# Optimization experiments

Measured on AMD Instinct MI355X. Metric: run time of the kernel, lower is better.

The kernel has to match this reference:

```python
import jax, jax.numpy as jnp
import numpy as np

D_MODEL = 512
N_HEADS = 8
D_K = D_MODEL // N_HEADS
B, L_Q, L_K = 4, 2048, 2048


def setup_inputs() -> dict:
    key = jax.random.key(0)
    ks = jax.random.split(key, 13)
    s = 1.0 / np.sqrt(D_MODEL)
    return {
        "Q_in": jax.random.normal(ks[0], (B, L_Q, D_MODEL), jnp.float32),
        "K_in": jax.random.normal(ks[1], (B, L_K, D_MODEL), jnp.float32),
        "V_in": jax.random.normal(ks[2], (B, L_K, D_MODEL), jnp.float32),
        "M": jax.random.uniform(ks[3], (N_HEADS, L_Q, L_K), jnp.float32),
        "Wq": jax.random.uniform(ks[4], (D_MODEL, D_MODEL), jnp.float32, -s, s),
        "bq": jnp.zeros((D_MODEL,), jnp.float32),
        "Wk": jax.random.uniform(ks[5], (D_MODEL, D_MODEL), jnp.float32, -s, s),
        "bk": jnp.zeros((D_MODEL,), jnp.float32),
        "Wv": jax.random.uniform(ks[6], (D_MODEL, D_MODEL), jnp.float32, -s, s),
        "bv": jnp.zeros((D_MODEL,), jnp.float32),
        "Wo": jax.random.uniform(ks[7], (D_MODEL, D_MODEL), jnp.float32, -s, s),
        "bo": jnp.zeros((D_MODEL,), jnp.float32),
        "logit_alpha": jnp.zeros((N_HEADS,), jnp.float32),
    }


def reference(Q_in, K_in, V_in, M, Wq, bq, Wk, bk, Wv, bv, Wo, bo, logit_alpha):
    b, lq, _ = Q_in.shape
    lk = K_in.shape[1]
    # projections (torch Linear: x @ W.T + b), split into heads: [b, h, l, d_k]
    Q = (Q_in @ Wq.T + bq).reshape(b, lq, N_HEADS, D_K).transpose(0, 2, 1, 3)
    K = (K_in @ Wk.T + bk).reshape(b, lk, N_HEADS, D_K).transpose(0, 2, 1, 3)
    V = (V_in @ Wv.T + bv).reshape(b, lk, N_HEADS, D_K).transpose(0, 2, 1, 3)
    logits = jnp.einsum("bhqd,bhkd->bhqk", Q, K) / jnp.sqrt(jnp.asarray(D_K, Q.dtype))
    attn = jax.nn.softmax(logits, axis=-1)
    alpha = jax.nn.sigmoid(logit_alpha)[None, :, None, None]  # [1, h, 1, 1]
    gate = alpha * M[None] + (1.0 - alpha)  # post-softmax soft-mask gate
    attn = attn * gate
    out = jnp.einsum("bhqk,bhkd->bqhd", attn, V).reshape(b, lq, D_MODEL)
    return out @ Wo.T + bo, attn
```

## Files before the change

### kernel.cpp

```cpp
#include <hip/hip_runtime.h>
#include <hip/hip_bf16.h>

typedef unsigned short u16;
typedef unsigned int u32;
typedef short bf16x8 __attribute__((ext_vector_type(8)));
typedef float f32x4 __attribute__((ext_vector_type(4)));
typedef u16 u16x8 __attribute__((ext_vector_type(8)));
typedef u32 u32x2 __attribute__((ext_vector_type(2)));

#define WQ_ 0
#define WK_ 262144
#define WV_ 524288
#define WO_ 786432
#define QP_ 1048576
#define KP_ (QP_ + 4194304)
#define VT_ (KP_ + 4194304)
#define OW_ (VT_ + 4194304)

#define C1F 0.18033688011112042f

__device__ __forceinline__ u16 f2bf(float f) {
  unsigned x = __float_as_uint(f);
  return (u16)((x + 0x7fffu + ((x >> 16) & 1u)) >> 16);
}

__device__ __forceinline__ u32 packbf2(float a, float b) {
  u32 lo = (u32)__bfloat16_as_ushort(__float2bfloat16(a));
  u32 hi = (u32)__bfloat16_as_ushort(__float2bfloat16(b));
  return lo | (hi << 16);
}

__device__ __forceinline__ void async16(const void* g, void* l) {
  __builtin_amdgcn_global_load_lds(
      (const __attribute__((address_space(1))) unsigned int*)g,
      (__attribute__((address_space(3))) unsigned int*)l, 16, 0, 0);
}

__global__ void convert_w(const float* __restrict__ Wq, const float* __restrict__ Wk,
                          const float* __restrict__ Wv, const float* __restrict__ Wo,
                          u16* __restrict__ ws) {
  int seg = blockIdx.y;
  const float* src = (seg == 0) ? Wq : (seg == 1) ? Wk : (seg == 2) ? Wv : Wo;
  u16* dst = ws + seg * 262144;
  int i = (blockIdx.x * 256 + threadIdx.x) * 8;
  float4 a = *(const float4*)(src + i);
  float4 b = *(const float4*)(src + i + 4);
  u16x8 o;
  o[0] = f2bf(a.x); o[1] = f2bf(a.y); o[2] = f2bf(a.z); o[3] = f2bf(a.w);
  o[4] = f2bf(b.x); o[5] = f2bf(b.y); o[6] = f2bf(b.z); o[7] = f2bf(b.w);
  *(u16x8*)(dst + i) = o;
}

template <int MODE>
__global__ __launch_bounds__(256, 3) void gemm_nt(
    const float* __restrict__ A0, const float* __restrict__ A1,
    const float* __restrict__ A2, u16* __restrict__ ws,
    const float* __restrict__ bias0, const float* __restrict__ bias1,
    const float* __restrict__ bias2, float* __restrict__ outF) {
  const int tid = threadIdx.x, lane = tid & 63, wave = tid >> 6;
  const int wm = wave >> 1, wn = wave & 1;
  const int z = blockIdx.z;
  const float* Af = (z == 0) ? A0 : (z == 1) ? A1 : A2;
  const u16* W = ws + (MODE == 0 ? z * 262144 : (int)WO_);
  const u16* Ab = ws + OW_;
  const float* bias = (z == 0) ? bias0 : (z == 1) ? bias1 : bias2;
  const int bm0 = blockIdx.y * 128, bn0 = blockIdx.x * 128;

  __shared__ u16 At[8192];
  __shared__ u16 Bt[8192];

  f32x4 acc[4][4];
#pragma unroll
  for (int i = 0; i < 4; ++i)
#pragma unroll
    for (int j = 0; j < 4; ++j) acc[i][j] = (f32x4){0.f, 0.f, 0.f, 0.f};

  const int grp16 = (lane >> 4) * 16;

  for (int kt = 0; kt < 8; ++kt) {
    __syncthreads();
#pragma unroll
    for (int c = 0; c < 4; ++c) {
      int o = wave * 4096 + c * 1024 + lane * 16;
      int row = o >> 7;
      int colb = (o & 127) ^ ((row & 7) << 4);
      async16((const char*)W + (size_t)(bn0 + row) * 1024 + kt * 128 + colb,
              (char*)Bt + wave * 4096 + c * 1024);
      if (MODE == 1) {
        async16((const char*)Ab + (size_t)(bm0 + row) * 1024 + kt * 128 + colb,
                (char*)At + wave * 4096 + c * 1024);
      }
    }
    if (MODE == 0) {
#pragma unroll
      for (int i = 0; i < 4; ++i) {
        int c = tid + 256 * i;
        int row = c >> 3, fc = (c & 7) * 8;
        const float* s = Af + (size_t)(bm0 + row) * 512 + kt * 64 + fc;
        f32x4 x0 = *(const f32x4*)s;
        f32x4 x1 = *(const f32x4*)(s + 4);
        u16x8 p;
        p[0] = __bfloat16_as_ushort(__float2bfloat16(x0[0]));
        p[1] = __bfloat16_as_ushort(__float2bfloat16(x0[1]));
        p[2] = __bfloat16_as_ushort(__float2bfloat16(x0[2]));
        p[3] = __bfloat16_as_ushort(__float2bfloat16(x0[3]));
        p[4] = __bfloat16_as_ushort(__float2bfloat16(x1[0]));
        p[5] = __bfloat16_as_ushort(__float2bfloat16(x1[1]));
        p[6] = __bfloat16_as_ushort(__float2bfloat16(x1[2]));
        p[7] = __bfloat16_as_ushort(__float2bfloat16(x1[3]));
        int db = row * 128 + ((fc * 2) ^ ((row & 7) << 4));
        *(u16x8*)((char*)At + db) = p;
      }
    }
    __syncthreads();
    bf16x8 af[4][2], bfr[4][2];
#pragma unroll
    for (int rb = 0; rb < 4; ++rb) {
      int row = wm * 64 + rb * 16 + (lane & 15);
      const char* base = (const char*)At + row * 128;
      int sw = (row & 7) << 4;
      af[rb][0] = *(const bf16x8*)(base + (grp16 ^ sw));
      af[rb][1] = *(const bf16x8*)(base + ((64 + grp16) ^ sw));
    }
#pragma unroll
    for (int cb = 0; cb < 4; ++cb) {
      int row = wn * 64 + cb * 16 + (lane & 15);
      const char* base = (const char*)Bt + row * 128;
      int sw = (row & 7) << 4;
      bfr[cb][0] = *(const bf16x8*)(base + (grp16 ^ sw));
      bfr[cb][1] = *(const bf16x8*)(base + ((64 + grp16) ^ sw));
    }
#pragma unroll
    for (int rb = 0; rb < 4; ++rb)
#pragma unroll
      for (int cb = 0; cb < 4; ++cb) {
        acc[rb][cb] = __builtin_amdgcn_mfma_f32_16x16x32_bf16(af[rb][0], bfr[cb][0],
                                                              acc[rb][cb], 0, 0, 0);
        acc[rb][cb] = __builtin_amdgcn_mfma_f32_16x16x32_bf16(af[rb][1], bfr[cb][1],
                                                              acc[rb][cb], 0, 0, 0);
      }
  }

#pragma unroll
  for (int rb = 0; rb < 4; ++rb) {
#pragma unroll
    for (int cb = 0; cb < 4; ++cb) {
      int col = bn0 + wn * 64 + cb * 16 + (lane & 15);
      float bvl = bias[col];
#pragma unroll
      for (int r = 0; r < 4; ++r) {
        int rr = bm0 + wm * 64 + rb * 16 + (lane >> 4) * 4 + r;
        float v = acc[rb][cb][r] + bvl;
        if (MODE == 1) {
          outF[(size_t)rr * 512 + col] = v;
        } else {
          int b = rr >> 11, q = rr & 2047, hh = col >> 6, dd = col & 63;
          int bh = (b << 3) | hh;
          if (z == 0) {
            ws[QP_ + (size_t)(bh * 2048 + q) * 64 + dd] = f2bf(v * C1F);
          } else if (z == 1) {
            ws[KP_ + (size_t)(bh * 2048 + q) * 64 + dd] = f2bf(v);
          } else {
            ws[VT_ + (size_t)bh * 131072 + (size_t)dd * 2048 + q] = f2bf(v);
          }
        }
      }
    }
  }
}

__global__ __launch_bounds__(256, 4) void attn_kernel(u16* __restrict__ ws,
                                                      const float* __restrict__ Mg,
                                                      const float* __restrict__ la,
                                                      float* __restrict__ attnOut) {
  const int tid = threadIdx.x, lane = tid & 63, wv = tid >> 6;
  const int colLane = lane & 15, grp = lane >> 4;
  const int yb = blockIdx.y, h = yb >> 2, b = yb & 3, bh = b * 8 + h;
  const int q0 = blockIdx.x * 64;
  const u16* Qp = ws + QP_ + (size_t)bh * 131072;
  const u16* Kp = ws + KP_ + (size_t)bh * 131072;
  const u16* Vtg = ws + VT_ + (size_t)bh * 131072;
  const float* Mh = Mg + (size_t)h * 4194304;
  float alpha = 1.f / (1.f + __expf(-la[h]));
  float oma = 1.f - alpha;

  __shared__ u16 Kt[2][4096];
  __shared__ u16 Vt[2][4096];
  __shared__ u16 Pl[4096];

  const int grp16 = grp * 16;

  bf16x8 qa0, qa1;
  {
    const u16* qb = Qp + (size_t)(q0 + wv * 16 + colLane) * 64;
    qa0 = *(const bf16x8*)(qb + grp * 8);
    qa1 = *(const bf16x8*)(qb + 32 + grp * 8);
  }

  auto stageK = [&](int buf, int kt) {
#pragma unroll
    for (int c = 0; c < 2; ++c) {
      int o = (wv * 2 + c) * 1024 + lane * 16;
      int srcb = o ^ (((o >> 7) & 7) << 4);
      async16((const char*)Kp + kt * 8192 + srcb,
              (char*)(Kt[buf]) + (wv * 2 + c) * 1024);
    }
  };
  auto stageV = [&](int buf, int kt) {
#pragma unroll
    for (int c = 0; c < 2; ++c) {
      int o = (wv * 2 + c) * 1024 + lane * 16;
      int d = o >> 7;
      int kb2 = (o & 127) ^ ((d & 7) << 4);
      async16((const char*)Vtg + (size_t)d * 4096 + kt * 128 + kb2,
              (char*)(Vt[buf]) + (wv * 2 + c) * 1024);
    }
  };
  auto qk = [&](const u16* Ktc, float sc[4][4]) {
#pragma unroll
    for (int cb = 0; cb < 4; ++cb) {
      int row = cb * 16 + colLane;
      const char* kb = (const char*)Ktc + row * 128;
      int sw = (row & 7) << 4;
      bf16x8 k0 = *(const bf16x8*)(kb + (grp16 ^ sw));
      bf16x8 k1 = *(const bf16x8*)(kb + ((64 + grp16) ^ sw));
      f32x4 a = (f32x4){0.f, 0.f, 0.f, 0.f};
      a = __builtin_amdgcn_mfma_f32_16x16x32_bf16(k0, qa0, a, 0, 0, 0);
      a = __builtin_amdgcn_mfma_f32_16x16x32_bf16(k1, qa1, a, 0, 0, 0);
#pragma unroll
      for (int r = 0; r < 4; ++r) sc[cb][r] = a[r];
    }
  };

  float zp = 0.f;
  stageK(0, 0);
  __syncthreads();
  int cur = 0;
  for (int kt = 0; kt < 32; ++kt) {
    if (kt < 31) stageK(cur ^ 1, kt + 1);
    float sc[4][4];
    qk(Kt[cur], sc);
#pragma unroll
    for (int cb = 0; cb < 4; ++cb)
#pragma unroll
      for (int r = 0; r < 4; ++r) zp += exp2f(sc[cb][r]);
    __syncthreads();
    cur ^= 1;
  }
  zp += __shfl_xor(zp, 16);
  zp += __shfl_xor(zp, 32);
  float invZ = 1.f / zp;
  float aZ = alpha * invZ, oZ = oma * invZ;

  f32x4 oacc[4];
#pragma unroll
  for (int d = 0; d < 4; ++d) oacc[d] = (f32x4){0.f, 0.f, 0.f, 0.f};

  const int qg = q0 + wv * 16 + colLane;
  const float* Mr = Mh + (size_t)qg * 2048 + grp * 4;
  float* Ar = attnOut + ((size_t)(bh * 2048 + qg)) * 2048 + grp * 4;
  char* pb = (char*)Pl + wv * 2048 + colLane * 128;
  const int psw = (colLane & 7) << 4;

  stageK(0, 0);
  stageV(0, 0);
  __syncthreads();
  cur = 0;
  for (int kt = 0; kt < 32; ++kt) {
    if (kt < 31) { stageK(cur ^ 1, kt + 1); stageV(cur ^ 1, kt + 1); }
    const float* Mk = Mr + kt * 64;
    float4 mreg[4];
#pragma unroll
    for (int cb = 0; cb < 4; ++cb) mreg[cb] = *(const float4*)(Mk + cb * 16);
    float sc[4][4];
    qk(Kt[cur], sc);
    float* Ak = Ar + kt * 64;
#pragma unroll
    for (int cb = 0; cb < 4; ++cb) {
      f32x4 uv;
      uv[0] = exp2f(sc[cb][0]) * fmaf(aZ, mreg[cb].x, oZ);
      uv[1] = exp2f(sc[cb][1]) * fmaf(aZ, mreg[cb].y, oZ);
      uv[2] = exp2f(sc[cb][2]) * fmaf(aZ, mreg[cb].z, oZ);
      uv[3] = exp2f(sc[cb][3]) * fmaf(aZ, mreg[cb].w, oZ);
      __builtin_nontemporal_store(uv, (f32x4*)(Ak + cb * 16));
      u32x2 pv;
      pv[0] = packbf2(uv[0], uv[1]);
      pv[1] = packbf2(uv[2], uv[3]);
      *(u32x2*)(pb + ((cb * 32 + grp * 8) ^ psw)) = pv;
    }
    bf16x8 pa0 = *(const bf16x8*)(pb + (grp16 ^ psw));
    bf16x8 pa1 = *(const bf16x8*)(pb + ((64 + grp16) ^ psw));
    const u16* Vtc = Vt[cur];
#pragma unroll
    for (int db = 0; db < 4; ++db) {
      int dcol = db * 16 + colLane;
      const char* vb = (const char*)Vtc + dcol * 128;
      int sw = (dcol & 7) << 4;
      bf16x8 v0 = *(const bf16x8*)(vb + (grp16 ^ sw));
      bf16x8 v1 = *(const bf16x8*)(vb + ((64 + grp16) ^ sw));
      oacc[db] = __builtin_amdgcn_mfma_f32_16x16x32_bf16(pa0, v0, oacc[db], 0, 0, 0);
      oacc[db] = __builtin_amdgcn_mfma_f32_16x16x32_bf16(pa1, v1, oacc[db], 0, 0, 0);
    }
    __syncthreads();
    cur ^= 1;
  }

#pragma unroll
  for (int db = 0; db < 4; ++db) {
    int dcol = db * 16 + colLane;
#pragma unroll
    for (int r = 0; r < 4; ++r) {
      int qq = q0 + wv * 16 + grp * 4 + r;
      ws[OW_ + (size_t)(b * 2048 + qq) * 512 + h * 64 + dcol] = f2bf(oacc[db][r]);
    }
  }
}

extern "C" void kernel_launch(void* const* d_in, const int* in_sizes, int n_in,
                              void* d_out, int out_size, void* d_ws, size_t ws_size,
                              hipStream_t stream) {
  const float* Qi = (const float*)d_in[0];
  const float* Ki = (const float*)d_in[1];
  const float* Vi = (const float*)d_in[2];
  const float* M = (const float*)d_in[3];
  const float* Wq = (const float*)d_in[4];
  const float* bq = (const float*)d_in[5];
  const float* Wk = (const float*)d_in[6];
  const float* bk = (const float*)d_in[7];
  const float* Wv = (const float*)d_in[8];
  const float* bv = (const float*)d_in[9];
  const float* Wo = (const float*)d_in[10];
  const float* bo = (const float*)d_in[11];
  const float* la = (const float*)d_in[12];
  u16* ws = (u16*)d_ws;
  float* outMain = (float*)d_out;
  float* outAttn = outMain + 4194304;

  convert_w<<<dim3(128, 4), 256, 0, stream>>>(Wq, Wk, Wv, Wo, ws);
  gemm_nt<0><<<dim3(4, 64, 3), 256, 0, stream>>>(Qi, Ki, Vi, ws, bq, bk, bv, nullptr);
  attn_kernel<<<dim3(32, 32), 256, 0, stream>>>(ws, M, la, outAttn);
  gemm_nt<1><<<dim3(4, 64, 1), 256, 0, stream>>>(nullptr, nullptr, nullptr, ws, bo,
                                                 nullptr, nullptr, outMain);
}
```

Baseline: 239.0 us.

## Split softmax denominator pass into separate larger-tile kernel and prefetch mask

Moves the first pass over K (computing the per-row softmax denominator) out of the attention kernel into a dedicated z_kernel. That kernel uses 512-thread blocks covering 128 queries with 128-key tiles, so each K tile staged into shared memory is reused across more queries, and it writes row sums to a workspace buffer. The attention kernel reads these sums and also software-prefetches the next mask tile into registers one iteration ahead. The cost is an extra kernel launch, a workspace round trip for Z, and more registers held live for the prefetched mask.

```diff
diff --git a/kernel.cpp b/kernel.cpp
--- a/kernel.cpp
+++ b/kernel.cpp
@@ -16,6 +16,7 @@
 #define KP_ (QP_ + 4194304)
 #define VT_ (KP_ + 4194304)
 #define OW_ (VT_ + 4194304)
+#define ZB_ (OW_ + 4194304)
 
 #define C1F 0.18033688011112042f
 
@@ -169,7 +170,61 @@
   }
 }
 
+__global__ __launch_bounds__(512, 2) void z_kernel(u16* __restrict__ ws,
+                                                   float* __restrict__ zb) {
+  const int tid = threadIdx.x, lane = tid & 63, wv = tid >> 6;
+  const int colLane = lane & 15, grp = lane >> 4;
+  const int bh = blockIdx.y;
+  const int q0 = blockIdx.x * 128;
+  const u16* Qp = ws + QP_ + (size_t)bh * 131072;
+  const u16* Kp = ws + KP_ + (size_t)bh * 131072;
+  __shared__ u16 Kt[2][8192];
+  const int grp16 = grp * 16;
+
+  bf16x8 qa0, qa1;
+  {
+    const u16* qb = Qp + (size_t)(q0 + wv * 16 + colLane) * 64;
+    qa0 = *(const bf16x8*)(qb + grp * 8);
+    qa1 = *(const bf16x8*)(qb + 32 + grp * 8);
+  }
+  auto stage = [&](int buf, int kt) {
+#pragma unroll
+    for (int c = 0; c < 2; ++c) {
+      int o = (c * 512 + tid) * 16;
+      int row = o >> 7;
+      int colb = (o & 127) ^ ((row & 7) << 4);
+      async16((const char*)Kp + kt * 16384 + row * 128 + colb,
+              (char*)(Kt[buf]) + o);
+    }
+  };
+  float zp = 0.f;
+  stage(0, 0);
+  __syncthreads();
+  int cur = 0;
+  for (int kt = 0; kt < 16; ++kt) {
+    if (kt < 15) stage(cur ^ 1, kt + 1);
+#pragma unroll
+    for (int cb = 0; cb < 8; ++cb) {
+      int row = cb * 16 + colLane;
+      const char* kb = (const char*)(Kt[cur]) + row * 128;
+      int sw = (row & 7) << 4;
+      bf16x8 k0 = *(const bf16x8*)(kb + (grp16 ^ sw));
+      bf16x8 k1 = *(const bf16x8*)(kb + ((64 + grp16) ^ sw));
+      f32x4 a = (f32x4){0.f, 0.f, 0.f, 0.f};
+      a = __builtin_amdgcn_mfma_f32_16x16x32_bf16(k0, qa0, a, 0, 0, 0);
+      a = __builtin_amdgcn_mfma_f32_16x16x32_bf16(k1, qa1, a, 0, 0, 0);
+      zp += exp2f(a[0]) + exp2f(a[1]) + exp2f(a[2]) + exp2f(a[3]);
+    }
+    __syncthreads();
+    cur ^= 1;
+  }
+  zp += __shfl_xor(zp, 16);
+  zp += __shfl_xor(zp, 32);
+  if (lane < 16) zb[(size_t)bh * 2048 + q0 + wv * 16 + colLane] = zp;
+}
+
 __global__ __launch_bounds__(256, 4) void attn_kernel(u16* __restrict__ ws,
+                                                      const float* __restrict__ zb,
                                                       const float* __restrict__ Mg,
                                                       const float* __restrict__ la,
                                                       float* __restrict__ attnOut) {
@@ -197,6 +252,10 @@
     qa1 = *(const bf16x8*)(qb + 32 + grp * 8);
   }
 
+  const int qg = q0 + wv * 16 + colLane;
+  float invZ = 1.f / zb[(size_t)bh * 2048 + qg];
+  float aZ = alpha * invZ, oZ = oma * invZ;
+
   auto stageK = [&](int buf, int kt) {
 #pragma unroll
     for (int c = 0; c < 2; ++c) {
@@ -232,56 +291,41 @@
     }
   };
 
-  float zp = 0.f;
-  stageK(0, 0);
-  __syncthreads();
-  int cur = 0;
-  for (int kt = 0; kt < 32; ++kt) {
-    if (kt < 31) stageK(cur ^ 1, kt + 1);
-    float sc[4][4];
-    qk(Kt[cur], sc);
-#pragma unroll
-    for (int cb = 0; cb < 4; ++cb)
-#pragma unroll
-      for (int r = 0; r < 4; ++r) zp += exp2f(sc[cb][r]);
-    __syncthreads();
-    cur ^= 1;
-  }
-  zp += __shfl_xor(zp, 16);
-  zp += __shfl_xor(zp, 32);
-  float invZ = 1.f / zp;
-  float aZ = alpha * invZ, oZ = oma * invZ;
-
   f32x4 oacc[4];
 #pragma unroll
   for (int d = 0; d < 4; ++d) oacc[d] = (f32x4){0.f, 0.f, 0.f, 0.f};
 
-  const int qg = q0 + wv * 16 + colLane;
   const float* Mr = Mh + (size_t)qg * 2048 + grp * 4;
   float* Ar = attnOut + ((size_t)(bh * 2048 + qg)) * 2048 + grp * 4;
   char* pb = (char*)Pl + wv * 2048 + colLane * 128;
   const int psw = (colLane & 7) << 4;
 
+  float4 mcur[4], mnxt[4];
+#pragma unroll
+  for (int cb = 0; cb < 4; ++cb) mcur[cb] = *(const float4*)(Mr + cb * 16);
+
   stageK(0, 0);
   stageV(0, 0);
   __syncthreads();
-  cur = 0;
+  int cur = 0;
   for (int kt = 0; kt < 32; ++kt) {
     if (kt < 31) { stageK(cur ^ 1, kt + 1); stageV(cur ^ 1, kt + 1); }
-    const float* Mk = Mr + kt * 64;
-    float4 mreg[4];
-#pragma unroll
-    for (int cb = 0; cb < 4; ++cb) mreg[cb] = *(const float4*)(Mk + cb * 16);
+    {
+      int ktn = (kt < 31) ? kt + 1 : 31;
+      const float* Mk = Mr + ktn * 64;
+#pragma unroll
+      for (int cb = 0; cb < 4; ++cb) mnxt[cb] = *(const float4*)(Mk + cb * 16);
+    }
     float sc[4][4];
     qk(Kt[cur], sc);
     float* Ak = Ar + kt * 64;
 #pragma unroll
     for (int cb = 0; cb < 4; ++cb) {
       f32x4 uv;
-      uv[0] = exp2f(sc[cb][0]) * fmaf(aZ, mreg[cb].x, oZ);
-      uv[1] = exp2f(sc[cb][1]) * fmaf(aZ, mreg[cb].y, oZ);
-      uv[2] = exp2f(sc[cb][2]) * fmaf(aZ, mreg[cb].z, oZ);
-      uv[3] = exp2f(sc[cb][3]) * fmaf(aZ, mreg[cb].w, oZ);
+      uv[0] = exp2f(sc[cb][0]) * fmaf(aZ, mcur[cb].x, oZ);
+      uv[1] = exp2f(sc[cb][1]) * fmaf(aZ, mcur[cb].y, oZ);
+      uv[2] = exp2f(sc[cb][2]) * fmaf(aZ, mcur[cb].z, oZ);
+      uv[3] = exp2f(sc[cb][3]) * fmaf(aZ, mcur[cb].w, oZ);
       __builtin_nontemporal_store(uv, (f32x4*)(Ak + cb * 16));
       u32x2 pv;
       pv[0] = packbf2(uv[0], uv[1]);
@@ -301,6 +345,8 @@
       oacc[db] = __builtin_amdgcn_mfma_f32_16x16x32_bf16(pa0, v0, oacc[db], 0, 0, 0);
       oacc[db] = __builtin_amdgcn_mfma_f32_16x16x32_bf16(pa1, v1, oacc[db], 0, 0, 0);
     }
+#pragma unroll
+    for (int cb = 0; cb < 4; ++cb) mcur[cb] = mnxt[cb];
     __syncthreads();
     cur ^= 1;
   }
@@ -333,12 +379,14 @@
   const float* bo = (const float*)d_in[11];
   const float* la = (const float*)d_in[12];
   u16* ws = (u16*)d_ws;
+  float* zb = (float*)(ws + ZB_);
   float* outMain = (float*)d_out;
   float* outAttn = outMain + 4194304;
 
   convert_w<<<dim3(128, 4), 256, 0, stream>>>(Wq, Wk, Wv, Wo, ws);
   gemm_nt<0><<<dim3(4, 64, 3), 256, 0, stream>>>(Qi, Ki, Vi, ws, bq, bk, bv, nullptr);
-  attn_kernel<<<dim3(32, 32), 256, 0, stream>>>(ws, M, la, outAttn);
+  z_kernel<<<dim3(16, 32), 512, 0, stream>>>(ws, zb);
+  attn_kernel<<<dim3(32, 32), 256, 0, stream>>>(ws, zb, M, la, outAttn);
   gemm_nt<1><<<dim3(4, 64, 1), 256, 0, stream>>>(nullptr, nullptr, nullptr, ws, bo,
                                                  nullptr, nullptr, outMain);
 }
```

New measurement: 269.2 us. +12.6%, slower.

## Load K and V fragments directly from global memory, dropping LDS staging

Applied to the files above, without the earlier changes.

Removes the double-buffered async LDS staging of K and V tiles along with the per-iteration block barriers. Each wave now loads its own MFMA operand fragments straight from global memory into registers. This drops barrier synchronisation and LDS traffic, but each of the four waves refetches the same K/V data and loses cross-wave sharing, which puts more load on L1/L2. The kernel is dominated by writing the attention matrix and reading the mask, so K/V reads may not be the bottleneck.

```diff
diff --git a/kernel.cpp b/kernel.cpp
--- a/kernel.cpp
+++ b/kernel.cpp
@@ -184,8 +184,6 @@
   float alpha = 1.f / (1.f + __expf(-la[h]));
   float oma = 1.f - alpha;
 
-  __shared__ u16 Kt[2][4096];
-  __shared__ u16 Vt[2][4096];
   __shared__ u16 Pl[4096];
 
   const int grp16 = grp * 16;
@@ -197,55 +195,32 @@
     qa1 = *(const bf16x8*)(qb + 32 + grp * 8);
   }
 
-  auto stageK = [&](int buf, int kt) {
-#pragma unroll
-    for (int c = 0; c < 2; ++c) {
-      int o = (wv * 2 + c) * 1024 + lane * 16;
-      int srcb = o ^ (((o >> 7) & 7) << 4);
-      async16((const char*)Kp + kt * 8192 + srcb,
-              (char*)(Kt[buf]) + (wv * 2 + c) * 1024);
+  auto qk = [&](int kt, float sc[4][4]) {
+    bf16x8 k0[4], k1[4];
+#pragma unroll
+    for (int cb = 0; cb < 4; ++cb) {
+      const u16* kb = Kp + (size_t)(kt * 64 + cb * 16 + colLane) * 64 + grp * 8;
+      k0[cb] = *(const bf16x8*)kb;
+      k1[cb] = *(const bf16x8*)(kb + 32);
+    }
+#pragma unroll
+    for (int cb = 0; cb < 4; ++cb) {
+      f32x4 a = (f32x4){0.f, 0.f, 0.f, 0.f};
+      a = __builtin_amdgcn_mfma_f32_16x16x32_bf16(k0[cb], qa0, a, 0, 0, 0);
+      a = __builtin_amdgcn_mfma_f32_16x16x32_bf16(k1[cb], qa1, a, 0, 0, 0);
+#pragma unroll
+      for (int r = 0; r < 4; ++r) sc[cb][r] = a[r];
     }
   };
-  auto stageV = [&](int buf, int kt) {
-#pragma unroll
-    for (int c = 0; c < 2; ++c) {
-      int o = (wv * 2 + c) * 1024 + lane * 16;
-      int d = o >> 7;
-      int kb2 = (o & 127) ^ ((d & 7) << 4);
-      async16((const char*)Vtg + (size_t)d * 4096 + kt * 128 + kb2,
-              (char*)(Vt[buf]) + (wv * 2 + c) * 1024);
-    }
-  };
-  auto qk = [&](const u16* Ktc, float sc[4][4]) {
-#pragma unroll
-    for (int cb = 0; cb < 4; ++cb) {
-      int row = cb * 16 + colLane;
-      const char* kb = (const char*)Ktc + row * 128;
-      int sw = (row & 7) << 4;
-      bf16x8 k0 = *(const bf16x8*)(kb + (grp16 ^ sw));
-      bf16x8 k1 = *(const bf16x8*)(kb + ((64 + grp16) ^ sw));
-      f32x4 a = (f32x4){0.f, 0.f, 0.f, 0.f};
-      a = __builtin_amdgcn_mfma_f32_16x16x32_bf16(k0, qa0, a, 0, 0, 0);
-      a = __builtin_amdgcn_mfma_f32_16x16x32_bf16(k1, qa1, a, 0, 0, 0);
-#pragma unroll
-      for (int r = 0; r < 4; ++r) sc[cb][r] = a[r];
-    }
-  };
 
   float zp = 0.f;
-  stageK(0, 0);
-  __syncthreads();
-  int cur = 0;
   for (int kt = 0; kt < 32; ++kt) {
-    if (kt < 31) stageK(cur ^ 1, kt + 1);
     float sc[4][4];
-    qk(Kt[cur], sc);
+    qk(kt, sc);
 #pragma unroll
     for (int cb = 0; cb < 4; ++cb)
 #pragma unroll
       for (int r = 0; r < 4; ++r) zp += exp2f(sc[cb][r]);
-    __syncthreads();
-    cur ^= 1;
   }
   zp += __shfl_xor(zp, 16);
   zp += __shfl_xor(zp, 32);
@@ -262,18 +237,13 @@
   char* pb = (char*)Pl + wv * 2048 + colLane * 128;
   const int psw = (colLane & 7) << 4;
 
-  stageK(0, 0);
-  stageV(0, 0);
-  __syncthreads();
-  cur = 0;
   for (int kt = 0; kt < 32; ++kt) {
-    if (kt < 31) { stageK(cur ^ 1, kt + 1); stageV(cur ^ 1, kt + 1); }
     const float* Mk = Mr + kt * 64;
     float4 mreg[4];
 #pragma unroll
     for (int cb = 0; cb < 4; ++cb) mreg[cb] = *(const float4*)(Mk + cb * 16);
     float sc[4][4];
-    qk(Kt[cur], sc);
+    qk(kt, sc);
     float* Ak = Ar + kt * 64;
 #pragma unroll
     for (int cb = 0; cb < 4; ++cb) {
@@ -290,19 +260,18 @@
     }
     bf16x8 pa0 = *(const bf16x8*)(pb + (grp16 ^ psw));
     bf16x8 pa1 = *(const bf16x8*)(pb + ((64 + grp16) ^ psw));
-    const u16* Vtc = Vt[cur];
+    bf16x8 v0[4], v1[4];
 #pragma unroll
     for (int db = 0; db < 4; ++db) {
-      int dcol = db * 16 + colLane;
-      const char* vb = (const char*)Vtc + dcol * 128;
-      int sw = (dcol & 7) << 4;
-      bf16x8 v0 = *(const bf16x8*)(vb + (grp16 ^ sw));
-      bf16x8 v1 = *(const bf16x8*)(vb + ((64 + grp16) ^ sw));
-      oacc[db] = __builtin_amdgcn_mfma_f32_16x16x32_bf16(pa0, v0, oacc[db], 0, 0, 0);
-      oacc[db] = __builtin_amdgcn_mfma_f32_16x16x32_bf16(pa1, v1, oacc[db], 0, 0, 0);
-    }
-    __syncthreads();
-    cur ^= 1;
+      const u16* vb = Vtg + (size_t)(db * 16 + colLane) * 2048 + kt * 64 + grp * 8;
+      v0[db] = *(const bf16x8*)vb;
+      v1[db] = *(const bf16x8*)(vb + 32);
+    }
+#pragma unroll
+    for (int db = 0; db < 4; ++db) {
+      oacc[db] = __builtin_amdgcn_mfma_f32_16x16x32_bf16(pa0, v0[db], oacc[db], 0, 0, 0);
+      oacc[db] = __builtin_amdgcn_mfma_f32_16x16x32_bf16(pa1, v1[db], oacc[db], 0, 0, 0);
+    }
   }
 
 #pragma unroll
```

After: 481.4 us. +101.4%, slower.
